# Performance work log

Hardware: AMD Instinct MI355X
Metric: run time of the kernel (lower is better)

Reference implementation:

```python
import jax, jax.numpy as jnp
import numpy as np

H = 16          # ATTENTION_HEAD
E = 300         # EXPANSION_LENGTH
D = 768         # TEXT_EMBEDDING_DIM
HD = D // H     # 48


def setup_inputs() -> dict:
    key = jax.random.key(0)
    ks = jax.random.split(key, 10)
    b, n, ql, kl = 1, 4, 64, 64
    q = jax.random.normal(ks[0], (b, n, ql, D), dtype=jnp.float32)
    k = jax.random.normal(ks[1], (b, 1, kl, D), dtype=jnp.float32)
    v = jax.random.normal(ks[2], (b, 1, kl, D), dtype=jnp.float32)
    s = 1.0 / np.sqrt(D)
    Wq = jax.random.normal(ks[3], (D, D), dtype=jnp.float32) * s
    bq = jnp.zeros((D,), dtype=jnp.float32)
    Wk = jax.random.normal(ks[4], (D, D), dtype=jnp.float32) * s
    bk = jnp.zeros((D,), dtype=jnp.float32)
    Wv = jax.random.normal(ks[5], (D, D), dtype=jnp.float32) * s
    bv = jnp.zeros((D,), dtype=jnp.float32)
    memory = jax.random.normal(ks[6], (1, E, H, HD), dtype=jnp.float32) * 0.05
    return {"q": q, "k": k, "v": v, "Wq": Wq, "bq": bq, "Wk": Wk,
            "bk": bk, "Wv": Wv, "bv": bv, "memory": memory}


def reference(q, k, v, Wq, bq, Wk, bk, Wv, bv, memory):
    b, n, ql, _ = q.shape
    kl = k.shape[2]
    # Dense projections
    Q = (q @ Wq + bq).reshape(b, n, ql, H, HD)          # bnqhd
    K = (k @ Wk + bk).reshape(b, kl, H, HD)             # bkhd
    V = (v @ Wv + bv).reshape(b, kl, H, HD)             # bkhd
    # memory (1,E,H,HD) -> (1,E,1,H,HD); K -> (b,1,kl,H,HD); broadcast sum
    broad_sum = memory[:, :, None, :, :] + K[:, None, :, :, :]   # bekhd
    M = jax.nn.relu(jnp.einsum('bekhd,bnqhd->bnekqh', broad_sum, Q))
    E_seq = jnp.einsum('bnekqh,bkhd->bnekhd', M, V)
    out = jnp.einsum('bnekhd,bnekqh->bnqhd', E_seq, M)
    return out.reshape(q.shape)
```

## Files before the change

### kernel.cpp

```cpp
#include <hip/hip_runtime.h>

#define H   16
#define E   300
#define D   768
#define HD  48
#define QL  64
#define KL  64
#define NH  64
#define ROWS 384
#define SPLITK 12
#define NCH 4

#define OFF_PP 0
#define OFF_PF (SPLITK*ROWS*D)
#define OFF_A  (OFF_PF + ROWS*D)
#define OFF_B  (OFF_A + NH*E*QL)
#define OFF_SP (OFF_B + NH*KL*QL)

__global__ __launch_bounds__(256, 2) void proj_kernel(
    const float* __restrict__ qin, const float* __restrict__ kin, const float* __restrict__ vin,
    const float* __restrict__ Wq, const float* __restrict__ Wk, const float* __restrict__ Wv,
    float* __restrict__ ws)
{
    const int rowblk = blockIdx.x;
    const int col0   = blockIdx.y * 128;
    const int ks     = blockIdx.z;
    const int kbase  = ks * 64;

    const float* W = (rowblk < 4) ? Wq : (rowblk == 4) ? Wk : Wv;

    __shared__ float XsT[32][68];
    __shared__ float Ws[32][128];

    const int tid = threadIdx.x;
    const int r0  = (tid >> 4) * 4;
    const int c0  = (tid & 15) * 8;

    float acc[4][8];
    #pragma unroll
    for (int i = 0; i < 4; i++)
        #pragma unroll
        for (int j = 0; j < 8; j++) acc[i][j] = 0.f;

    for (int kk2 = 0; kk2 < 64; kk2 += 32) {
        #pragma unroll
        for (int it = 0; it < 2; it++) {
            const int idx = it * 256 + tid;
            const int row = idx >> 3;
            const int d4  = (idx & 7) * 4;
            const int grow = rowblk * 64 + row;
            const float* src = (grow < 256) ? (qin + grow * D)
                             : (grow < 320) ? (kin + (grow - 256) * D)
                                            : (vin + (grow - 320) * D);
            const float4 xv = *(const float4*)(src + kbase + kk2 + d4);
            XsT[d4 + 0][row] = xv.x; XsT[d4 + 1][row] = xv.y;
            XsT[d4 + 2][row] = xv.z; XsT[d4 + 3][row] = xv.w;
        }
        #pragma unroll
        for (int it = 0; it < 4; it++) {
            const int idx = it * 256 + tid;
            const int dk  = idx >> 5;
            const int c4  = (idx & 31) * 4;
            *(float4*)&Ws[dk][c4] =
                *(const float4*)(W + (kbase + kk2 + dk) * D + col0 + c4);
        }
        __syncthreads();
        #pragma unroll
        for (int dk = 0; dk < 32; dk++) {
            const float4 x0 = *(const float4*)&XsT[dk][r0];
            const float4 w0 = *(const float4*)&Ws[dk][c0];
            const float4 w1 = *(const float4*)&Ws[dk][c0 + 4];
            const float xr[4] = {x0.x, x0.y, x0.z, x0.w};
            const float wc[8] = {w0.x, w0.y, w0.z, w0.w, w1.x, w1.y, w1.z, w1.w};
            #pragma unroll
            for (int i = 0; i < 4; i++)
                #pragma unroll
                for (int j = 0; j < 8; j++)
                    acc[i][j] = fmaf(xr[i], wc[j], acc[i][j]);
        }
        __syncthreads();
    }
    float* P = ws + OFF_PP + ks * (ROWS * D);
    #pragma unroll
    for (int i = 0; i < 4; i++) {
        float* base = P + (rowblk * 64 + r0 + i) * D + col0 + c0;
        *(float4*)(base)     = make_float4(acc[i][0], acc[i][1], acc[i][2], acc[i][3]);
        *(float4*)(base + 4) = make_float4(acc[i][4], acc[i][5], acc[i][6], acc[i][7]);
    }
}

__global__ __launch_bounds__(256) void reduce_kernel(
    const float* __restrict__ bq, const float* __restrict__ bk, const float* __restrict__ bv,
    float* __restrict__ ws)
{
    const int idx = (blockIdx.x * 256 + threadIdx.x) * 4;
    const float* PP = ws + OFF_PP;
    float4 v = *(const float4*)(PP + idx);
    #pragma unroll
    for (int c = 1; c < SPLITK; c++) {
        const float4 p = *(const float4*)(PP + c * (ROWS * D) + idx);
        v.x += p.x; v.y += p.y; v.z += p.z; v.w += p.w;
    }
    const int row = idx / D, col = idx % D;
    const float* bias = (row < 256) ? bq : (row < 320) ? bk : bv;
    const float4 b = *(const float4*)(bias + col);
    v.x += b.x; v.y += b.y; v.z += b.z; v.w += b.w;
    *(float4*)(ws + OFF_PF + idx) = v;
}

__global__ __launch_bounds__(256) void ab_kernel(
    const float* __restrict__ memo, float* __restrict__ ws)
{
    const int nh = blockIdx.x;
    const int rg = blockIdx.y;
    const int n = nh >> 4, h = nh & 15;
    const float* Pf = ws + OFF_PF;
    float* A = ws + OFF_A;
    float* B = ws + OFF_B;

    __shared__ float RsT[48][132];
    __shared__ float QsT[48][68];

    const int tid = threadIdx.x;
    #pragma unroll
    for (int it = 0; it < 6; it++) {
        const int idx = it * 256 + tid;
        const int row = idx / 12;
        const int d4  = (idx % 12) * 4;
        const int rr = rg * 128 + row;
        float4 rv = make_float4(0.f, 0.f, 0.f, 0.f);
        if (rr < E)            rv = *(const float4*)(memo + rr * D + h * HD + d4);
        else if (rr < E + KL)  rv = *(const float4*)(Pf + (256 + rr - E) * D + h * HD + d4);
        RsT[d4 + 0][row] = rv.x; RsT[d4 + 1][row] = rv.y;
        RsT[d4 + 2][row] = rv.z; RsT[d4 + 3][row] = rv.w;
    }
    #pragma unroll
    for (int it = 0; it < 3; it++) {
        const int idx = it * 256 + tid;
        const int q  = idx / 12;
        const int d4 = (idx % 12) * 4;
        const float4 qv = *(const float4*)(Pf + (n * QL + q) * D + h * HD + d4);
        QsT[d4 + 0][q] = qv.x; QsT[d4 + 1][q] = qv.y;
        QsT[d4 + 2][q] = qv.z; QsT[d4 + 3][q] = qv.w;
    }
    __syncthreads();

    const int r0 = (tid >> 4) * 8;
    const int q0 = (tid & 15) * 4;
    float acc[8][4];
    #pragma unroll
    for (int i = 0; i < 8; i++)
        #pragma unroll
        for (int j = 0; j < 4; j++) acc[i][j] = 0.f;

    #pragma unroll 4
    for (int d = 0; d < HD; d++) {
        const float4 rf0 = *(const float4*)&RsT[d][r0];
        const float4 rf1 = *(const float4*)&RsT[d][r0 + 4];
        const float4 qf  = *(const float4*)&QsT[d][q0];
        const float rr8[8] = {rf0.x, rf0.y, rf0.z, rf0.w, rf1.x, rf1.y, rf1.z, rf1.w};
        const float qq4[4] = {qf.x, qf.y, qf.z, qf.w};
        #pragma unroll
        for (int i = 0; i < 8; i++)
            #pragma unroll
            for (int j = 0; j < 4; j++)
                acc[i][j] = fmaf(rr8[i], qq4[j], acc[i][j]);
    }
    #pragma unroll
    for (int i = 0; i < 8; i++) {
        const int rr = rg * 128 + r0 + i;
        const float4 av = make_float4(acc[i][0], acc[i][1], acc[i][2], acc[i][3]);
        if (rr < E)            *(float4*)(A + (nh * E + rr) * QL + q0) = av;
        else if (rr < E + KL)  *(float4*)(B + (nh * KL + (rr - E)) * QL + q0) = av;
    }
}

__global__ __launch_bounds__(256, 1) void main_kernel(float* __restrict__ ws)
{
    const int nh = blockIdx.x;
    const int eg = blockIdx.y;
    const int tid = threadIdx.x;
    const int lane = tid & 63;
    const int w = tid >> 6;

    __shared__ union {
        struct { float As[75 * 64]; float Bs[64][68]; } a;
        struct { float r0[64 * 64]; float r1[64 * 64]; } r;
    } sh;

    const float* Ag = ws + OFF_A + (nh * E + eg * 75) * QL;
    for (int idx = tid; idx < 1200; idx += 256)
        *(float4*)&sh.a.As[idx * 4] = *(const float4*)(Ag + idx * 4);
    const float* Bg = ws + OFF_B + nh * (KL * QL);
    #pragma unroll
    for (int it = 0; it < 4; it++) {
        const int idx = it * 256 + tid;
        const int k  = idx >> 4;
        const int q4 = (idx & 15) * 4;
        *(float4*)&sh.a.Bs[k][q4] = *(const float4*)(Bg + idx * 4);
    }
    __syncthreads();

    float b[64];
    #pragma unroll
    for (int j = 0; j < 16; j++)
        *(float4*)&b[j * 4] = *(const float4*)&sh.a.Bs[lane][j * 4];

    float s[64];
    #pragma unroll
    for (int j = 0; j < 64; j++) s[j] = 0.f;

    const int eBeg = w * 19;
    const int eEnd = (eBeg + 19 < 75) ? eBeg + 19 : 75;
    for (int e = eBeg; e < eEnd; e++) {
        float m[64];
        #pragma unroll
        for (int j4 = 0; j4 < 16; j4++) {
            const float4 a = *(const float4*)&sh.a.As[e * 64 + j4 * 4];
            m[j4 * 4 + 0] = fmaxf(a.x + b[j4 * 4 + 0], 0.f);
            m[j4 * 4 + 1] = fmaxf(a.y + b[j4 * 4 + 1], 0.f);
            m[j4 * 4 + 2] = fmaxf(a.z + b[j4 * 4 + 2], 0.f);
            m[j4 * 4 + 3] = fmaxf(a.w + b[j4 * 4 + 3], 0.f);
        }
        float p0 = 0.f, p1 = 0.f, p2 = 0.f, p3 = 0.f;
        #pragma unroll
        for (int j4 = 0; j4 < 16; j4++) {
            p0 += m[j4 * 4 + 0]; p1 += m[j4 * 4 + 1];
            p2 += m[j4 * 4 + 2]; p3 += m[j4 * 4 + 3];
        }
        const float p = (p0 + p1) + (p2 + p3);
        #pragma unroll
        for (int j = 0; j < 64; j++)
            s[j] = fmaf(m[j], p, s[j]);
    }

    __syncthreads();
    if (w >= 2) {
        float* red = (w == 2) ? sh.r.r0 : sh.r.r1;
        #pragma unroll
        for (int q = 0; q < 64; q++) red[q * 64 + lane] = s[q];
    }
    __syncthreads();
    if (w == 0) {
        #pragma unroll
        for (int q = 0; q < 64; q++) s[q] += sh.r.r0[q * 64 + lane];
    } else if (w == 1) {
        #pragma unroll
        for (int q = 0; q < 64; q++) s[q] += sh.r.r1[q * 64 + lane];
    }
    __syncthreads();
    if (w == 1) {
        #pragma unroll
        for (int q = 0; q < 64; q++) sh.r.r0[q * 64 + lane] = s[q];
    }
    __syncthreads();
    if (w == 0) {
        float* Sp = ws + OFF_SP + ((eg * NH + nh) * QL) * KL;
        #pragma unroll
        for (int q = 0; q < 64; q++)
            Sp[q * KL + lane] = s[q] + sh.r.r0[q * 64 + lane];
    }
}

__global__ __launch_bounds__(256) void out_kernel(
    const float* __restrict__ ws_c, float* __restrict__ outp)
{
    const int nh = blockIdx.x;
    const int qq = blockIdx.y;
    const int n = nh >> 4, h = nh & 15;
    const int q0 = qq * 16;
    const float* Sp = ws_c + OFF_SP;
    const float* Pf = ws_c + OFF_PF;

    __shared__ float S_l[16][64];
    __shared__ float V_l[64][52];

    const int tid = threadIdx.x;
    #pragma unroll
    for (int it = 0; it < 4; it++) {
        const int idx = it * 256 + tid;
        const int qi = idx >> 6, k = idx & 63;
        float sum = 0.f;
        #pragma unroll
        for (int c = 0; c < NCH; c++)
            sum += Sp[((c * NH + nh) * QL + q0 + qi) * KL + k];
        S_l[qi][k] = sum;
    }
    #pragma unroll
    for (int it = 0; it < 3; it++) {
        const int idx = it * 256 + tid;
        const int k  = idx / 12;
        const int d4 = (idx % 12) * 4;
        *(float4*)&V_l[k][d4] = *(const float4*)(Pf + (320 + k) * D + h * HD + d4);
    }
    __syncthreads();

    const int qi = tid >> 4;
    const int dg = tid & 15;
    if (dg < 12) {
        float a0 = 0.f, a1 = 0.f, a2 = 0.f, a3 = 0.f;
        #pragma unroll 8
        for (int k = 0; k < KL; k++) {
            const float sv = S_l[qi][k];
            const float4 vf = *(const float4*)&V_l[k][dg * 4];
            a0 = fmaf(sv, vf.x, a0); a1 = fmaf(sv, vf.y, a1);
            a2 = fmaf(sv, vf.z, a2); a3 = fmaf(sv, vf.w, a3);
        }
        *(float4*)(outp + (n * QL + q0 + qi) * D + h * HD + dg * 4) =
            make_float4(a0, a1, a2, a3);
    }
}

extern "C" void kernel_launch(void* const* d_in, const int* in_sizes, int n_in,
                              void* d_out, int out_size, void* d_ws, size_t ws_size,
                              hipStream_t stream)
{
    const float* q    = (const float*)d_in[0];
    const float* k    = (const float*)d_in[1];
    const float* v    = (const float*)d_in[2];
    const float* Wq   = (const float*)d_in[3];
    const float* bq   = (const float*)d_in[4];
    const float* Wk   = (const float*)d_in[5];
    const float* bk   = (const float*)d_in[6];
    const float* Wv   = (const float*)d_in[7];
    const float* bv   = (const float*)d_in[8];
    const float* memo = (const float*)d_in[9];
    float* ws   = (float*)d_ws;
    float* outp = (float*)d_out;

    hipLaunchKernelGGL(proj_kernel, dim3(6, 6, 12), dim3(256), 0, stream,
                       q, k, v, Wq, Wk, Wv, ws);
    hipLaunchKernelGGL(reduce_kernel, dim3(288), dim3(256), 0, stream, bq, bk, bv, ws);
    hipLaunchKernelGGL(ab_kernel, dim3(64, 3), dim3(256), 0, stream, memo, ws);
    hipLaunchKernelGGL(main_kernel, dim3(64, 4), dim3(256), 0, stream, ws);
    hipLaunchKernelGGL(out_kernel, dim3(64, 4), dim3(256), 0, stream, ws, outp);
}
```

Baseline: 121.8 us.

## Fuse split-K reduction into consumers and split attention work across more blocks

Removes the separate reduce kernel and instead sums the twelve split-K partials plus bias directly inside ab_kernel (for Q and K) and out_kernel (for V). It also halves the row tile in ab_kernel so the grid doubles, and cuts main_kernel's E chunk from 75 to 38 rows, doubling its grid and allowing two blocks per CU, with NCH raised to 8 to match. The aim is to drop a launch and a full write/read of the reduced projections, and to improve occupancy on a GPU with many CUs. The cost is redundant partial-sum reads, since each Q/K/V element is reduced by several blocks, and a larger Sp buffer for out_kernel to sum.

```diff
diff --git a/kernel.cpp b/kernel.cpp
--- a/kernel.cpp
+++ b/kernel.cpp
@@ -9,11 +9,11 @@
 #define NH  64
 #define ROWS 384
 #define SPLITK 12
-#define NCH 4
+#define NCH 8
+#define ECH 38
 
 #define OFF_PP 0
-#define OFF_PF (SPLITK*ROWS*D)
-#define OFF_A  (OFF_PF + ROWS*D)
+#define OFF_A  (SPLITK*ROWS*D)
 #define OFF_B  (OFF_A + NH*E*QL)
 #define OFF_SP (OFF_B + NH*KL*QL)
 
@@ -89,48 +89,40 @@
     }
 }
 
-__global__ __launch_bounds__(256) void reduce_kernel(
-    const float* __restrict__ bq, const float* __restrict__ bk, const float* __restrict__ bv,
-    float* __restrict__ ws)
-{
-    const int idx = (blockIdx.x * 256 + threadIdx.x) * 4;
-    const float* PP = ws + OFF_PP;
-    float4 v = *(const float4*)(PP + idx);
-    #pragma unroll
-    for (int c = 1; c < SPLITK; c++) {
-        const float4 p = *(const float4*)(PP + c * (ROWS * D) + idx);
-        v.x += p.x; v.y += p.y; v.z += p.z; v.w += p.w;
-    }
-    const int row = idx / D, col = idx % D;
-    const float* bias = (row < 256) ? bq : (row < 320) ? bk : bv;
-    const float4 b = *(const float4*)(bias + col);
-    v.x += b.x; v.y += b.y; v.z += b.z; v.w += b.w;
-    *(float4*)(ws + OFF_PF + idx) = v;
-}
-
 __global__ __launch_bounds__(256) void ab_kernel(
-    const float* __restrict__ memo, float* __restrict__ ws)
+    const float* __restrict__ memo, const float* __restrict__ bq,
+    const float* __restrict__ bk, float* __restrict__ ws)
 {
     const int nh = blockIdx.x;
     const int rg = blockIdx.y;
     const int n = nh >> 4, h = nh & 15;
-    const float* Pf = ws + OFF_PF;
+    const float* PP = ws + OFF_PP;
     float* A = ws + OFF_A;
     float* B = ws + OFF_B;
 
-    __shared__ float RsT[48][132];
+    __shared__ float RsT[48][68];
     __shared__ float QsT[48][68];
 
     const int tid = threadIdx.x;
     #pragma unroll
-    for (int it = 0; it < 6; it++) {
+    for (int it = 0; it < 3; it++) {
         const int idx = it * 256 + tid;
         const int row = idx / 12;
         const int d4  = (idx % 12) * 4;
-        const int rr = rg * 128 + row;
+        const int rr = rg * 64 + row;
         float4 rv = make_float4(0.f, 0.f, 0.f, 0.f);
-        if (rr < E)            rv = *(const float4*)(memo + rr * D + h * HD + d4);
-        else if (rr < E + KL)  rv = *(const float4*)(Pf + (256 + rr - E) * D + h * HD + d4);
+        if (rr < E) {
+            rv = *(const float4*)(memo + rr * D + h * HD + d4);
+        } else if (rr < E + KL) {
+            const int prow = 256 + (rr - E);
+            #pragma unroll
+            for (int c = 0; c < SPLITK; c++) {
+                const float4 p = *(const float4*)(PP + c * (ROWS * D) + prow * D + h * HD + d4);
+                rv.x += p.x; rv.y += p.y; rv.z += p.z; rv.w += p.w;
+            }
+            const float4 bb = *(const float4*)(bk + h * HD + d4);
+            rv.x += bb.x; rv.y += bb.y; rv.z += bb.z; rv.w += bb.w;
+        }
         RsT[d4 + 0][row] = rv.x; RsT[d4 + 1][row] = rv.y;
         RsT[d4 + 2][row] = rv.z; RsT[d4 + 3][row] = rv.w;
     }
@@ -139,57 +131,66 @@
         const int idx = it * 256 + tid;
         const int q  = idx / 12;
         const int d4 = (idx % 12) * 4;
-        const float4 qv = *(const float4*)(Pf + (n * QL + q) * D + h * HD + d4);
+        const int prow = n * QL + q;
+        float4 qv = make_float4(0.f, 0.f, 0.f, 0.f);
+        #pragma unroll
+        for (int c = 0; c < SPLITK; c++) {
+            const float4 p = *(const float4*)(PP + c * (ROWS * D) + prow * D + h * HD + d4);
+            qv.x += p.x; qv.y += p.y; qv.z += p.z; qv.w += p.w;
+        }
+        const float4 bb = *(const float4*)(bq + h * HD + d4);
+        qv.x += bb.x; qv.y += bb.y; qv.z += bb.z; qv.w += bb.w;
         QsT[d4 + 0][q] = qv.x; QsT[d4 + 1][q] = qv.y;
         QsT[d4 + 2][q] = qv.z; QsT[d4 + 3][q] = qv.w;
     }
     __syncthreads();
 
-    const int r0 = (tid >> 4) * 8;
+    const int r0 = (tid >> 4) * 4;
     const int q0 = (tid & 15) * 4;
-    float acc[8][4];
-    #pragma unroll
-    for (int i = 0; i < 8; i++)
+    float acc[4][4];
+    #pragma unroll
+    for (int i = 0; i < 4; i++)
         #pragma unroll
         for (int j = 0; j < 4; j++) acc[i][j] = 0.f;
 
     #pragma unroll 4
     for (int d = 0; d < HD; d++) {
-        const float4 rf0 = *(const float4*)&RsT[d][r0];
-        const float4 rf1 = *(const float4*)&RsT[d][r0 + 4];
-        const float4 qf  = *(const float4*)&QsT[d][q0];
-        const float rr8[8] = {rf0.x, rf0.y, rf0.z, rf0.w, rf1.x, rf1.y, rf1.z, rf1.w};
+        const float4 rf = *(const float4*)&RsT[d][r0];
+        const float4 qf = *(const float4*)&QsT[d][q0];
+        const float rr4[4] = {rf.x, rf.y, rf.z, rf.w};
         const float qq4[4] = {qf.x, qf.y, qf.z, qf.w};
         #pragma unroll
-        for (int i = 0; i < 8; i++)
+        for (int i = 0; i < 4; i++)
             #pragma unroll
             for (int j = 0; j < 4; j++)
-                acc[i][j] = fmaf(rr8[i], qq4[j], acc[i][j]);
-    }
-    #pragma unroll
-    for (int i = 0; i < 8; i++) {
-        const int rr = rg * 128 + r0 + i;
+                acc[i][j] = fmaf(rr4[i], qq4[j], acc[i][j]);
+    }
+    #pragma unroll
+    for (int i = 0; i < 4; i++) {
+        const int rr = rg * 64 + r0 + i;
         const float4 av = make_float4(acc[i][0], acc[i][1], acc[i][2], acc[i][3]);
         if (rr < E)            *(float4*)(A + (nh * E + rr) * QL + q0) = av;
         else if (rr < E + KL)  *(float4*)(B + (nh * KL + (rr - E)) * QL + q0) = av;
     }
 }
 
-__global__ __launch_bounds__(256, 1) void main_kernel(float* __restrict__ ws)
+__global__ __launch_bounds__(256, 2) void main_kernel(float* __restrict__ ws)
 {
     const int nh = blockIdx.x;
     const int eg = blockIdx.y;
+    const int e0 = eg * ECH;
+    const int ecnt = (E - e0 < ECH) ? (E - e0) : ECH;
     const int tid = threadIdx.x;
     const int lane = tid & 63;
     const int w = tid >> 6;
 
     __shared__ union {
-        struct { float As[75 * 64]; float Bs[64][68]; } a;
+        struct { float As[ECH * 64]; float Bs[64][68]; } a;
         struct { float r0[64 * 64]; float r1[64 * 64]; } r;
     } sh;
 
-    const float* Ag = ws + OFF_A + (nh * E + eg * 75) * QL;
-    for (int idx = tid; idx < 1200; idx += 256)
+    const float* Ag = ws + OFF_A + (nh * E + e0) * QL;
+    for (int idx = tid; idx < ecnt * 16; idx += 256)
         *(float4*)&sh.a.As[idx * 4] = *(const float4*)(Ag + idx * 4);
     const float* Bg = ws + OFF_B + nh * (KL * QL);
     #pragma unroll
@@ -210,8 +211,8 @@
     #pragma unroll
     for (int j = 0; j < 64; j++) s[j] = 0.f;
 
-    const int eBeg = w * 19;
-    const int eEnd = (eBeg + 19 < 75) ? eBeg + 19 : 75;
+    const int eBeg = (ecnt * w) >> 2;
+    const int eEnd = (ecnt * (w + 1)) >> 2;
     for (int e = eBeg; e < eEnd; e++) {
         float m[64];
         #pragma unroll
@@ -263,14 +264,15 @@
 }
 
 __global__ __launch_bounds__(256) void out_kernel(
-    const float* __restrict__ ws_c, float* __restrict__ outp)
+    const float* __restrict__ bv, const float* __restrict__ ws_c,
+    float* __restrict__ outp)
 {
     const int nh = blockIdx.x;
     const int qq = blockIdx.y;
     const int n = nh >> 4, h = nh & 15;
     const int q0 = qq * 16;
     const float* Sp = ws_c + OFF_SP;
-    const float* Pf = ws_c + OFF_PF;
+    const float* PP = ws_c + OFF_PP;
 
     __shared__ float S_l[16][64];
     __shared__ float V_l[64][52];
@@ -291,7 +293,16 @@
         const int idx = it * 256 + tid;
         const int k  = idx / 12;
         const int d4 = (idx % 12) * 4;
-        *(float4*)&V_l[k][d4] = *(const float4*)(Pf + (320 + k) * D + h * HD + d4);
+        const int prow = 320 + k;
+        float4 vv = make_float4(0.f, 0.f, 0.f, 0.f);
+        #pragma unroll
+        for (int c = 0; c < SPLITK; c++) {
+            const float4 p = *(const float4*)(PP + c * (ROWS * D) + prow * D + h * HD + d4);
+            vv.x += p.x; vv.y += p.y; vv.z += p.z; vv.w += p.w;
+        }
+        const float4 bb = *(const float4*)(bv + h * HD + d4);
+        vv.x += bb.x; vv.y += bb.y; vv.z += bb.z; vv.w += bb.w;
+        *(float4*)&V_l[k][d4] = vv;
     }
     __syncthreads();
 
@@ -330,8 +341,7 @@
 
     hipLaunchKernelGGL(proj_kernel, dim3(6, 6, 12), dim3(256), 0, stream,
                        q, k, v, Wq, Wk, Wv, ws);
-    hipLaunchKernelGGL(reduce_kernel, dim3(288), dim3(256), 0, stream, bq, bk, bv, ws);
-    hipLaunchKernelGGL(ab_kernel, dim3(64, 3), dim3(256), 0, stream, memo, ws);
-    hipLaunchKernelGGL(main_kernel, dim3(64, 4), dim3(256), 0, stream, ws);
-    hipLaunchKernelGGL(out_kernel, dim3(64, 4), dim3(256), 0, stream, ws, outp);
-}
+    hipLaunchKernelGGL(ab_kernel, dim3(64, 6), dim3(256), 0, stream, memo, bq, bk, ws);
+    hipLaunchKernelGGL(main_kernel, dim3(64, 8), dim3(256), 0, stream, ws);
+    hipLaunchKernelGGL(out_kernel, dim3(64, 4), dim3(256), 0, stream, bv, ws, outp);
+}
```

After: 122.1 us. Within noise of the previous version (+0.2%).

## Fuse A/B score, main accumulation and V projection into one kernel

Applied to the files above, without the earlier changes.

Merges the ab, main and out kernels into a single mega_kernel that computes the memory·Q and K·Q scores in shared memory, runs the relu/accumulate loop, then applies V per e-chunk. It writes partial outputs per e-chunk, which a small outsum kernel then reduces. E is split into 8 chunks of 38 instead of 4 chunks of 75, giving more blocks and occupancy 2. This removes two launches and the global round-trips for the A, B and S intermediates. The cost is recomputing K·Q and V·S in every chunk block and adding a reduction over 8 partials.

```diff
diff --git a/kernel.cpp b/kernel.cpp
--- a/kernel.cpp
+++ b/kernel.cpp
@@ -9,13 +9,12 @@
 #define NH  64
 #define ROWS 384
 #define SPLITK 12
-#define NCH 4
+#define NEG 8
+#define ECH 38
 
 #define OFF_PP 0
 #define OFF_PF (SPLITK*ROWS*D)
-#define OFF_A  (OFF_PF + ROWS*D)
-#define OFF_B  (OFF_A + NH*E*QL)
-#define OFF_SP (OFF_B + NH*KL*QL)
+#define OFF_OP (OFF_PF + ROWS*D)
 
 __global__ __launch_bounds__(256, 2) void proj_kernel(
     const float* __restrict__ qin, const float* __restrict__ kin, const float* __restrict__ vin,
@@ -108,115 +107,131 @@
     *(float4*)(ws + OFF_PF + idx) = v;
 }
 
-__global__ __launch_bounds__(256) void ab_kernel(
+__global__ __launch_bounds__(256, 2) void mega_kernel(
     const float* __restrict__ memo, float* __restrict__ ws)
-{
-    const int nh = blockIdx.x;
-    const int rg = blockIdx.y;
-    const int n = nh >> 4, h = nh & 15;
-    const float* Pf = ws + OFF_PF;
-    float* A = ws + OFF_A;
-    float* B = ws + OFF_B;
-
-    __shared__ float RsT[48][132];
-    __shared__ float QsT[48][68];
-
-    const int tid = threadIdx.x;
-    #pragma unroll
-    for (int it = 0; it < 6; it++) {
-        const int idx = it * 256 + tid;
-        const int row = idx / 12;
-        const int d4  = (idx % 12) * 4;
-        const int rr = rg * 128 + row;
-        float4 rv = make_float4(0.f, 0.f, 0.f, 0.f);
-        if (rr < E)            rv = *(const float4*)(memo + rr * D + h * HD + d4);
-        else if (rr < E + KL)  rv = *(const float4*)(Pf + (256 + rr - E) * D + h * HD + d4);
-        RsT[d4 + 0][row] = rv.x; RsT[d4 + 1][row] = rv.y;
-        RsT[d4 + 2][row] = rv.z; RsT[d4 + 3][row] = rv.w;
-    }
-    #pragma unroll
-    for (int it = 0; it < 3; it++) {
-        const int idx = it * 256 + tid;
-        const int q  = idx / 12;
-        const int d4 = (idx % 12) * 4;
-        const float4 qv = *(const float4*)(Pf + (n * QL + q) * D + h * HD + d4);
-        QsT[d4 + 0][q] = qv.x; QsT[d4 + 1][q] = qv.y;
-        QsT[d4 + 2][q] = qv.z; QsT[d4 + 3][q] = qv.w;
-    }
-    __syncthreads();
-
-    const int r0 = (tid >> 4) * 8;
-    const int q0 = (tid & 15) * 4;
-    float acc[8][4];
-    #pragma unroll
-    for (int i = 0; i < 8; i++)
-        #pragma unroll
-        for (int j = 0; j < 4; j++) acc[i][j] = 0.f;
-
-    #pragma unroll 4
-    for (int d = 0; d < HD; d++) {
-        const float4 rf0 = *(const float4*)&RsT[d][r0];
-        const float4 rf1 = *(const float4*)&RsT[d][r0 + 4];
-        const float4 qf  = *(const float4*)&QsT[d][q0];
-        const float rr8[8] = {rf0.x, rf0.y, rf0.z, rf0.w, rf1.x, rf1.y, rf1.z, rf1.w};
-        const float qq4[4] = {qf.x, qf.y, qf.z, qf.w};
-        #pragma unroll
-        for (int i = 0; i < 8; i++)
-            #pragma unroll
-            for (int j = 0; j < 4; j++)
-                acc[i][j] = fmaf(rr8[i], qq4[j], acc[i][j]);
-    }
-    #pragma unroll
-    for (int i = 0; i < 8; i++) {
-        const int rr = rg * 128 + r0 + i;
-        const float4 av = make_float4(acc[i][0], acc[i][1], acc[i][2], acc[i][3]);
-        if (rr < E)            *(float4*)(A + (nh * E + rr) * QL + q0) = av;
-        else if (rr < E + KL)  *(float4*)(B + (nh * KL + (rr - E)) * QL + q0) = av;
-    }
-}
-
-__global__ __launch_bounds__(256, 1) void main_kernel(float* __restrict__ ws)
 {
     const int nh = blockIdx.x;
     const int eg = blockIdx.y;
+    const int e0 = eg * ECH;
+    const int ecnt = (E - e0 < ECH) ? (E - e0) : ECH;
+    const int n = nh >> 4, h = nh & 15;
     const int tid = threadIdx.x;
     const int lane = tid & 63;
     const int w = tid >> 6;
 
-    __shared__ union {
-        struct { float As[75 * 64]; float Bs[64][68]; } a;
-        struct { float r0[64 * 64]; float r1[64 * 64]; } r;
-    } sh;
-
-    const float* Ag = ws + OFF_A + (nh * E + eg * 75) * QL;
-    for (int idx = tid; idx < 1200; idx += 256)
-        *(float4*)&sh.a.As[idx * 4] = *(const float4*)(Ag + idx * 4);
-    const float* Bg = ws + OFF_B + nh * (KL * QL);
-    #pragma unroll
-    for (int it = 0; it < 4; it++) {
+    const float* Pf = ws + OFF_PF;
+
+    __shared__ float As[ECH * 64];
+    __shared__ float Bs[64][68];
+    __shared__ float U[8832];
+
+    float* QsT = U;
+    float* KsT = U + 48 * 68;
+    float* MsT = U + 2 * 48 * 68;
+
+    #pragma unroll
+    for (int it = 0; it < 3; it++) {
         const int idx = it * 256 + tid;
-        const int k  = idx >> 4;
-        const int q4 = (idx & 15) * 4;
-        *(float4*)&sh.a.Bs[k][q4] = *(const float4*)(Bg + idx * 4);
+        const int r  = idx / 12;
+        const int d4 = (idx % 12) * 4;
+        const float4 qv = *(const float4*)(Pf + (n * QL + r) * D + h * HD + d4);
+        QsT[(d4 + 0) * 68 + r] = qv.x; QsT[(d4 + 1) * 68 + r] = qv.y;
+        QsT[(d4 + 2) * 68 + r] = qv.z; QsT[(d4 + 3) * 68 + r] = qv.w;
+        const float4 kv = *(const float4*)(Pf + (256 + r) * D + h * HD + d4);
+        KsT[(d4 + 0) * 68 + r] = kv.x; KsT[(d4 + 1) * 68 + r] = kv.y;
+        KsT[(d4 + 2) * 68 + r] = kv.z; KsT[(d4 + 3) * 68 + r] = kv.w;
+    }
+    for (int idx = tid; idx < ecnt * 12; idx += 256) {
+        const int e  = idx / 12;
+        const int d4 = (idx % 12) * 4;
+        const float4 mv = *(const float4*)(memo + (e0 + e) * D + h * HD + d4);
+        MsT[(d4 + 0) * 40 + e] = mv.x; MsT[(d4 + 1) * 40 + e] = mv.y;
+        MsT[(d4 + 2) * 40 + e] = mv.z; MsT[(d4 + 3) * 40 + e] = mv.w;
+    }
+    __syncthreads();
+
+    {
+        const int k0 = (tid >> 4) * 4;
+        const int q0 = (tid & 15) * 4;
+        float acc[4][4];
+        #pragma unroll
+        for (int i = 0; i < 4; i++)
+            #pragma unroll
+            for (int j = 0; j < 4; j++) acc[i][j] = 0.f;
+        #pragma unroll 4
+        for (int d = 0; d < HD; d++) {
+            const float4 kf = *(const float4*)&KsT[d * 68 + k0];
+            const float4 qf = *(const float4*)&QsT[d * 68 + q0];
+            const float kk4[4] = {kf.x, kf.y, kf.z, kf.w};
+            const float qq4[4] = {qf.x, qf.y, qf.z, qf.w};
+            #pragma unroll
+            for (int i = 0; i < 4; i++)
+                #pragma unroll
+                for (int j = 0; j < 4; j++)
+                    acc[i][j] = fmaf(kk4[i], qq4[j], acc[i][j]);
+        }
+        #pragma unroll
+        for (int i = 0; i < 4; i++)
+            *(float4*)&Bs[k0 + i][q0] =
+                make_float4(acc[i][0], acc[i][1], acc[i][2], acc[i][3]);
+    }
+    {
+        const int et = (tid >> 4) * 3;
+        const int q0 = (tid & 15) * 4;
+        float acc[3][4];
+        #pragma unroll
+        for (int i = 0; i < 3; i++)
+            #pragma unroll
+            for (int j = 0; j < 4; j++) acc[i][j] = 0.f;
+        #pragma unroll 4
+        for (int d = 0; d < HD; d++) {
+            const float me0 = MsT[d * 40 + et + 0];
+            const float me1 = MsT[d * 40 + et + 1];
+            const float me2 = MsT[d * 40 + et + 2];
+            const float4 qf = *(const float4*)&QsT[d * 68 + q0];
+            const float mm3[3] = {me0, me1, me2};
+            const float qq4[4] = {qf.x, qf.y, qf.z, qf.w};
+            #pragma unroll
+            for (int i = 0; i < 3; i++)
+                #pragma unroll
+                for (int j = 0; j < 4; j++)
+                    acc[i][j] = fmaf(mm3[i], qq4[j], acc[i][j]);
+        }
+        #pragma unroll
+        for (int i = 0; i < 3; i++)
+            if (et + i < ecnt)
+                *(float4*)&As[(et + i) * 64 + q0] =
+                    make_float4(acc[i][0], acc[i][1], acc[i][2], acc[i][3]);
     }
     __syncthreads();
 
     float b[64];
     #pragma unroll
     for (int j = 0; j < 16; j++)
-        *(float4*)&b[j * 4] = *(const float4*)&sh.a.Bs[lane][j * 4];
+        *(float4*)&b[j * 4] = *(const float4*)&Bs[lane][j * 4];
+    __syncthreads();
+
+    float* Vs = &Bs[0][0];
+    #pragma unroll
+    for (int it = 0; it < 3; it++) {
+        const int idx = it * 256 + tid;
+        const int k  = idx / 12;
+        const int d4 = (idx % 12) * 4;
+        const float4 vv = *(const float4*)(Pf + (320 + k) * D + h * HD + d4);
+        *(float4*)&Vs[k * 52 + d4] = vv;
+    }
 
     float s[64];
     #pragma unroll
     for (int j = 0; j < 64; j++) s[j] = 0.f;
 
-    const int eBeg = w * 19;
-    const int eEnd = (eBeg + 19 < 75) ? eBeg + 19 : 75;
+    const int eBeg = (ecnt * w) >> 2;
+    const int eEnd = (ecnt * (w + 1)) >> 2;
     for (int e = eBeg; e < eEnd; e++) {
         float m[64];
         #pragma unroll
         for (int j4 = 0; j4 < 16; j4++) {
-            const float4 a = *(const float4*)&sh.a.As[e * 64 + j4 * 4];
+            const float4 a = *(const float4*)&As[e * 64 + j4 * 4];
             m[j4 * 4 + 0] = fmaxf(a.x + b[j4 * 4 + 0], 0.f);
             m[j4 * 4 + 1] = fmaxf(a.y + b[j4 * 4 + 1], 0.f);
             m[j4 * 4 + 2] = fmaxf(a.z + b[j4 * 4 + 2], 0.f);
@@ -234,81 +249,79 @@
             s[j] = fmaf(m[j], p, s[j]);
     }
 
+    float* r0 = U;
+    float* r1 = U + 4096;
+    float* Ss = U + 4096;
     __syncthreads();
     if (w >= 2) {
-        float* red = (w == 2) ? sh.r.r0 : sh.r.r1;
+        float* red = (w == 2) ? r0 : r1;
         #pragma unroll
         for (int q = 0; q < 64; q++) red[q * 64 + lane] = s[q];
     }
     __syncthreads();
     if (w == 0) {
         #pragma unroll
-        for (int q = 0; q < 64; q++) s[q] += sh.r.r0[q * 64 + lane];
+        for (int q = 0; q < 64; q++) s[q] += r0[q * 64 + lane];
     } else if (w == 1) {
         #pragma unroll
-        for (int q = 0; q < 64; q++) s[q] += sh.r.r1[q * 64 + lane];
+        for (int q = 0; q < 64; q++) s[q] += r1[q * 64 + lane];
     }
     __syncthreads();
     if (w == 1) {
         #pragma unroll
-        for (int q = 0; q < 64; q++) sh.r.r0[q * 64 + lane] = s[q];
+        for (int q = 0; q < 64; q++) r0[q * 64 + lane] = s[q];
     }
     __syncthreads();
     if (w == 0) {
-        float* Sp = ws + OFF_SP + ((eg * NH + nh) * QL) * KL;
         #pragma unroll
         for (int q = 0; q < 64; q++)
-            Sp[q * KL + lane] = s[q] + sh.r.r0[q * 64 + lane];
-    }
-}
-
-__global__ __launch_bounds__(256) void out_kernel(
-    const float* __restrict__ ws_c, float* __restrict__ outp)
-{
-    const int nh = blockIdx.x;
-    const int qq = blockIdx.y;
-    const int n = nh >> 4, h = nh & 15;
-    const int q0 = qq * 16;
-    const float* Sp = ws_c + OFF_SP;
-    const float* Pf = ws_c + OFF_PF;
-
-    __shared__ float S_l[16][64];
-    __shared__ float V_l[64][52];
-
-    const int tid = threadIdx.x;
-    #pragma unroll
-    for (int it = 0; it < 4; it++) {
-        const int idx = it * 256 + tid;
-        const int qi = idx >> 6, k = idx & 63;
-        float sum = 0.f;
-        #pragma unroll
-        for (int c = 0; c < NCH; c++)
-            sum += Sp[((c * NH + nh) * QL + q0 + qi) * KL + k];
-        S_l[qi][k] = sum;
-    }
-    #pragma unroll
-    for (int it = 0; it < 3; it++) {
-        const int idx = it * 256 + tid;
-        const int k  = idx / 12;
-        const int d4 = (idx % 12) * 4;
-        *(float4*)&V_l[k][d4] = *(const float4*)(Pf + (320 + k) * D + h * HD + d4);
-    }
-    __syncthreads();
-
-    const int qi = tid >> 4;
-    const int dg = tid & 15;
-    if (dg < 12) {
-        float a0 = 0.f, a1 = 0.f, a2 = 0.f, a3 = 0.f;
+            Ss[q * 68 + lane] = s[q] + r0[q * 64 + lane];
+    }
+    __syncthreads();
+
+    {
+        const int q  = tid >> 2;
+        const int dg = tid & 3;
+        float4 a0 = make_float4(0.f, 0.f, 0.f, 0.f);
+        float4 a1 = a0, a2 = a0;
         #pragma unroll 8
         for (int k = 0; k < KL; k++) {
-            const float sv = S_l[qi][k];
-            const float4 vf = *(const float4*)&V_l[k][dg * 4];
-            a0 = fmaf(sv, vf.x, a0); a1 = fmaf(sv, vf.y, a1);
-            a2 = fmaf(sv, vf.z, a2); a3 = fmaf(sv, vf.w, a3);
-        }
-        *(float4*)(outp + (n * QL + q0 + qi) * D + h * HD + dg * 4) =
-            make_float4(a0, a1, a2, a3);
-    }
+            const float sv = Ss[q * 68 + k];
+            const float4 v0 = *(const float4*)&Vs[k * 52 + dg * 12 + 0];
+            const float4 v1 = *(const float4*)&Vs[k * 52 + dg * 12 + 4];
+            const float4 v2 = *(const float4*)&Vs[k * 52 + dg * 12 + 8];
+            a0.x = fmaf(sv, v0.x, a0.x); a0.y = fmaf(sv, v0.y, a0.y);
+            a0.z = fmaf(sv, v0.z, a0.z); a0.w = fmaf(sv, v0.w, a0.w);
+            a1.x = fmaf(sv, v1.x, a1.x); a1.y = fmaf(sv, v1.y, a1.y);
+            a1.z = fmaf(sv, v1.z, a1.z); a1.w = fmaf(sv, v1.w, a1.w);
+            a2.x = fmaf(sv, v2.x, a2.x); a2.y = fmaf(sv, v2.y, a2.y);
+            a2.z = fmaf(sv, v2.z, a2.z); a2.w = fmaf(sv, v2.w, a2.w);
+        }
+        float* OP = ws + OFF_OP + (((eg * NH) + nh) * QL + q) * 48 + dg * 12;
+        *(float4*)(OP + 0) = a0;
+        *(float4*)(OP + 4) = a1;
+        *(float4*)(OP + 8) = a2;
+    }
+}
+
+__global__ __launch_bounds__(256) void outsum_kernel(
+    const float* __restrict__ ws_c, float* __restrict__ outp)
+{
+    const int g = blockIdx.x * 256 + threadIdx.x;
+    const int d12 = g % 12;
+    const int q   = (g / 12) & 63;
+    const int nh  = g / 768;
+    const int n = nh >> 4, h = nh & 15;
+    const float* OP = ws_c + OFF_OP;
+
+    float4 acc = make_float4(0.f, 0.f, 0.f, 0.f);
+    #pragma unroll
+    for (int c = 0; c < NEG; c++) {
+        const float4 p = *(const float4*)(OP + c * (NH * QL * 48)
+                                          + (nh * QL + q) * 48 + d12 * 4);
+        acc.x += p.x; acc.y += p.y; acc.z += p.z; acc.w += p.w;
+    }
+    *(float4*)(outp + (n * QL + q) * D + h * HD + d12 * 4) = acc;
 }
 
 extern "C" void kernel_launch(void* const* d_in, const int* in_sizes, int n_in,
@@ -331,7 +344,6 @@
     hipLaunchKernelGGL(proj_kernel, dim3(6, 6, 12), dim3(256), 0, stream,
                        q, k, v, Wq, Wk, Wv, ws);
     hipLaunchKernelGGL(reduce_kernel, dim3(288), dim3(256), 0, stream, bq, bk, bv, ws);
-    hipLaunchKernelGGL(ab_kernel, dim3(64, 3), dim3(256), 0, stream, memo, ws);
-    hipLaunchKernelGGL(main_kernel, dim3(64, 4), dim3(256), 0, stream, ws);
-    hipLaunchKernelGGL(out_kernel, dim3(64, 4), dim3(256), 0, stream, ws, outp);
-}
+    hipLaunchKernelGGL(mega_kernel, dim3(64, NEG), dim3(256), 0, stream, memo, ws);
+    hipLaunchKernelGGL(outsum_kernel, dim3(192), dim3(256), 0, stream, ws, outp);
+}
```

Measured after the change: 117.0 us, median of 2. 3.9% less time.
